# Kernel tuning notes

Hardware: AMD Instinct MI355X
Metric: run time of the kernel (lower is better)

Reference implementation:

```python
import jax, jax.numpy as jnp
import numpy as np

N = 50000          # num graph nodes
E = 800000         # edges per direction
NGRAM, ODIM = 4, 32
DIMS = [128, 128, 64]
CLASSES = 128
MAXPE = 10
L2_EPS = 1e-12


def setup_inputs() -> dict:
    key = jax.random.key(0)
    ks = iter(jax.random.split(key, 40))
    d = {}
    d['x'] = jax.random.normal(next(ks), (N, DIMS[0]), jnp.float32)
    d['edge_index_in'] = jax.random.randint(next(ks), (2, E), 0, N, dtype=jnp.int64)
    d['edge_weight_in'] = jax.random.uniform(next(ks), (E,), jnp.float32)
    d['edge_index_out'] = jax.random.randint(next(ks), (2, E), 0, N, dtype=jnp.int64)
    d['edge_weight_out'] = jax.random.uniform(next(ks), (E,), jnp.float32)
    d['pe_table'] = jax.random.normal(next(ks), (MAXPE, ODIM), jnp.float32) * 0.05
    # per-layer DirectGCNLayer params (weights stored [in,out], i.e. torch W.T)
    for l in range(2):
        di, do = DIMS[l], DIMS[l + 1]
        s = 1.0 / np.sqrt(di)
        d[f'W_main_in_{l}'] = jax.random.normal(next(ks), (di, do), jnp.float32) * s
        d[f'W_main_out_{l}'] = jax.random.normal(next(ks), (di, do), jnp.float32) * s
        d[f'W_shared_{l}'] = jax.random.normal(next(ks), (di, do), jnp.float32) * s
        d[f'b_main_in_{l}'] = jnp.zeros((do,), jnp.float32)
        d[f'b_main_out_{l}'] = jnp.zeros((do,), jnp.float32)
        d[f'b_shared_in_{l}'] = jnp.zeros((do,), jnp.float32)
        d[f'b_shared_out_{l}'] = jnp.zeros((do,), jnp.float32)
        d[f'C_in_{l}'] = jnp.ones((N, 1), jnp.float32)
        d[f'C_out_{l}'] = jnp.ones((N, 1), jnp.float32)
    # residual projection for layer 1 (128 -> 64); layer 0 is identity
    d['res_W_1'] = jax.random.normal(next(ks), (DIMS[1], DIMS[2]), jnp.float32) * (1.0 / np.sqrt(DIMS[1]))
    d['res_b_1'] = jnp.zeros((DIMS[2],), jnp.float32)
    d['dec_W'] = jax.random.normal(next(ks), (DIMS[2], CLASSES), jnp.float32) * (1.0 / np.sqrt(DIMS[2]))
    d['dec_b'] = jnp.zeros((CLASSES,), jnp.float32)
    return d


def _prop(xW, ei, ew):
    # gather source, scale by edge weight, scatter-add to target (PyG aggr='add')
    return jax.ops.segment_sum(ew[:, None] * xW[ei[0]], ei[1], num_segments=N)


def _layer(h, ei_in, ew_in, ei_out, ew_out,
           Wmi, Wmo, Ws, bmi, bmo, bsi, bso, cin, cout):
    xs = h @ Ws  # shared transform, propagated over both edge sets
    ic = _prop(h @ Wmi, ei_in, ew_in) + bmi + _prop(xs, ei_in, ew_in) + bsi
    oc = _prop(h @ Wmo, ei_out, ew_out) + bmo + _prop(xs, ei_out, ew_out) + bso
    return cin * ic + cout * oc


def reference(x, edge_index_in, edge_weight_in, edge_index_out, edge_weight_out,
              pe_table,
              W_main_in_0, W_main_out_0, W_shared_0, b_main_in_0, b_main_out_0,
              b_shared_in_0, b_shared_out_0, C_in_0, C_out_0,
              W_main_in_1, W_main_out_1, W_shared_1, b_main_in_1, b_main_out_1,
              b_shared_in_1, b_shared_out_1, C_in_1, C_out_1,
              res_W_1, res_b_1, dec_W, dec_b):
    # positional encoding: add pe[:n_gram_len] to each n-gram slot
    h = (x.reshape(N, NGRAM, ODIM) + pe_table[:NGRAM][None]).reshape(N, NGRAM * ODIM)
    # layer 0 (identity residual); dropout p=0 / eval -> no-op
    h = jnp.tanh(_layer(h, edge_index_in, edge_weight_in, edge_index_out, edge_weight_out,
                        W_main_in_0, W_main_out_0, W_shared_0, b_main_in_0, b_main_out_0,
                        b_shared_in_0, b_shared_out_0, C_in_0, C_out_0) + h)
    # layer 1 (linear residual projection 128 -> 64)
    h = jnp.tanh(_layer(h, edge_index_in, edge_weight_in, edge_index_out, edge_weight_out,
                        W_main_in_1, W_main_out_1, W_shared_1, b_main_in_1, b_main_out_1,
                        b_shared_in_1, b_shared_out_1, C_in_1, C_out_1)
                 + h @ res_W_1 + res_b_1)
    logits = h @ dec_W + dec_b
    logp = jax.nn.log_softmax(logits, axis=-1)
    emb = h / (jnp.linalg.norm(h, axis=1, keepdims=True) + L2_EPS)
    return logp, emb
```

## Files before the change

kernel.cpp:

```cpp
#include <hip/hip_runtime.h>
#include <hip/hip_bf16.h>
#include <math.h>

typedef __hip_bfloat16  bf16;
typedef __hip_bfloat162 bf162;
typedef __attribute__((ext_vector_type(8))) short short8;
typedef __attribute__((ext_vector_type(4))) float floatx4;

#define BSZ     128
#define NBMAX   512
#define PACHUNK 8192

__device__ inline float4 bf4_to_f4(uint2 v) {
  float2 lo = __bfloat1622float2(*(bf162*)&v.x);
  float2 hi = __bfloat1622float2(*(bf162*)&v.y);
  return make_float4(lo.x, lo.y, hi.x, hi.y);
}
__device__ inline uint2 f4_to_bf4(float4 v) {
  bf162 lo = __float22bfloat162_rn(make_float2(v.x, v.y));
  bf162 hi = __float22bfloat162_rn(make_float2(v.z, v.w));
  uint2 r;
  r.x = *(unsigned*)&lo;
  r.y = *(unsigned*)&hi;
  return r;
}

__global__ __launch_bounds__(256) void k_bhist(const int* __restrict__ eiIn, const int* __restrict__ eiOut,
                                               int E, int* __restrict__ bcnt, int NB) {
  __shared__ int h[NBMAX];
  const int t = threadIdx.x;
  const int set = blockIdx.y;
  const int* dst = (set ? eiOut : eiIn) + E;
  for (int i = t; i < NB; i += 256) h[i] = 0;
  __syncthreads();
  const int base = blockIdx.x * PACHUNK;
  const int m = min(PACHUNK, E - base);
  #pragma unroll 4
  for (int r = 0; r < PACHUNK / 256; ++r) {
    int i = r * 256 + t;
    if (i < m) atomicAdd(&h[dst[base + i] >> 7], 1);
  }
  __syncthreads();
  for (int i = t; i < NB; i += 256) {
    int c = h[i];
    if (c) atomicAdd(&bcnt[set * NBMAX + i], c);
  }
}

__global__ __launch_bounds__(64) void k_bscan(const int* __restrict__ bcnt,
                                              int* __restrict__ BO, int* __restrict__ bcur, int NB) {
  const int set = blockIdx.x;
  const int t = threadIdx.x;
  int carry = 0;
  for (int base = 0; base < NB; base += 64) {
    int idx = base + t;
    int v = (idx < NB) ? bcnt[set * NBMAX + idx] : 0;
    int incl = v;
    #pragma unroll
    for (int d = 1; d < 64; d <<= 1) {
      int u = __shfl_up(incl, d, 64);
      if (t >= d) incl += u;
    }
    if (idx < NB) {
      int e = carry + incl - v;
      BO[set * NBMAX + idx]   = e;
      bcur[set * NBMAX + idx] = e;
    }
    carry += __shfl(incl, 63, 64);
  }
}

__global__ __launch_bounds__(256) void k_partA(const int* __restrict__ eiIn, const float* __restrict__ ewIn,
                                               const int* __restrict__ eiOut, const float* __restrict__ ewOut,
                                               int E, int* __restrict__ bucketCur,
                                               int2* __restrict__ sI, int2* __restrict__ sO, int NB) {
  __shared__ int2 staged[PACHUNK];
  __shared__ int cnt[NBMAX];
  __shared__ int sb[NBMAX];
  const int t = threadIdx.x;
  const int set = blockIdx.y;
  const int*   ei = set ? eiOut : eiIn;
  const float* ew = set ? ewOut : ewIn;
  int2* stg  = set ? sO : sI;
  int*  bcur = bucketCur + set * NBMAX;
  const int base = blockIdx.x * PACHUNK;
  const int m = min(PACHUNK, E - base);
  for (int b = t; b < NB; b += 256) cnt[b] = 0;
  __syncthreads();
  #pragma unroll 4
  for (int r = 0; r < PACHUNK / 256; ++r) {
    int i = r * 256 + t;
    if (i < m) atomicAdd(&cnt[ei[E + base + i] >> 7], 1);
  }
  __syncthreads();
  if (t < 64) {
    int carry = 0;
    int nch = (NB + 63) >> 6;
    for (int c = 0; c < nch; ++c) {
      int idx = c * 64 + t;
      int v = (idx < NB) ? cnt[idx] : 0;
      int incl = v;
      #pragma unroll
      for (int d = 1; d < 64; d <<= 1) {
        int u = __shfl_up(incl, d, 64);
        if (t >= d) incl += u;
      }
      if (idx < NB) sb[idx] = carry + incl - v;
      carry += __shfl(incl, 63, 64);
    }
  }
  __syncthreads();
  for (int b = t; b < NB; b += 256) {
    int c = cnt[b];
    if (c > 0) cnt[b] = atomicAdd(&bcur[b], c) - sb[b];
  }
  __syncthreads();
  #pragma unroll 4
  for (int r = 0; r < PACHUNK / 256; ++r) {
    int i = r * 256 + t;
    if (i < m) {
      int src = ei[base + i];
      int dst = ei[E + base + i];
      float w = ew[base + i];
      int b = dst >> 7;
      int rank = atomicAdd(&sb[b], 1);
      staged[rank] = make_int2(src | ((dst & 127) << 16) | (b << 23), __float_as_int(w));
    }
  }
  __syncthreads();
  #pragma unroll 4
  for (int r = 0; r < PACHUNK / 256; ++r) {
    int j = r * 256 + t;
    if (j < m) {
      int2 p = staged[j];
      int b = ((unsigned)p.x) >> 23;
      stg[cnt[b] + j] = p;
    }
  }
}

__global__ __launch_bounds__(256) void k_partB(const int* __restrict__ BO, const int* __restrict__ bcur,
                                               const int2* __restrict__ sI, const int2* __restrict__ sO,
                                               int2* __restrict__ eI, int2* __restrict__ eO,
                                               int* __restrict__ offsI, int* __restrict__ offsO, int N) {
  __shared__ int cnt[BSZ];
  __shared__ int excl[BSZ];
  __shared__ int cur[BSZ];
  const int t = threadIdx.x;
  const int b = blockIdx.x;
  const int set = blockIdx.y;
  const int2* stg = set ? sO : sI;
  int2* out = set ? eO : eI;
  int*  offs = set ? offsO : offsI;
  const int nlo = b << 7;
  const int nodes = min(BSZ, N - nlo);
  const int lo = BO[set * NBMAX + b];
  const int hi = bcur[set * NBMAX + b];
  if (t < BSZ) cnt[t] = 0;
  __syncthreads();
  for (int i = lo + t; i < hi; i += 256) atomicAdd(&cnt[(stg[i].x >> 16) & 127], 1);
  __syncthreads();
  if (t < 64) {
    int v0 = cnt[t];
    int i0 = v0;
    #pragma unroll
    for (int d = 1; d < 64; d <<= 1) { int u = __shfl_up(i0, d, 64); if (t >= d) i0 += u; }
    int v1 = cnt[64 + t];
    int i1 = v1;
    #pragma unroll
    for (int d = 1; d < 64; d <<= 1) { int u = __shfl_up(i1, d, 64); if (t >= d) i1 += u; }
    int tot0 = __shfl(i0, 63, 64);
    excl[t]      = i0 - v0;
    excl[64 + t] = tot0 + i1 - v1;
  }
  __syncthreads();
  if (t < BSZ) cur[t] = lo + excl[t];
  if (t < nodes) offs[nlo + t] = lo + excl[t];
  if (b == gridDim.x - 1 && t == 0) offs[N] = hi;
  __syncthreads();
  for (int i = lo + t; i < hi; i += 256) {
    int2 p = stg[i];
    int dl = (p.x >> 16) & 127;
    int pos = atomicAdd(&cur[dl], 1);
    out[pos] = make_int2(p.x & 0xffff, p.y);
  }
}

__device__ inline void pack_one(const float* __restrict__ W, bf16* __restrict__ P,
                                int id, int NT, int DO) {
  int lane = id & 63;
  int tile = id >> 6;
  int nt = tile % NT, kt = tile / NT;
  int col  = nt * 16 + (lane & 15);
  int krow = kt * 32 + (lane >> 4) * 8;
  bf16* dst = P + (size_t)id * 8;
  #pragma unroll
  for (int j = 0; j < 8; ++j) dst[j] = __float2bfloat16(W[(size_t)(krow + j) * DO + col]);
}
__global__ void k_packall(const float* __restrict__ Wmi0, const float* __restrict__ Wmo0,
                          const float* __restrict__ Ws0,
                          const float* __restrict__ Wmi1, const float* __restrict__ Wmo1,
                          const float* __restrict__ Ws1,
                          const float* __restrict__ resW, const float* __restrict__ Wd,
                          const float* __restrict__ bmi0, const float* __restrict__ bsi0,
                          const float* __restrict__ bmo0, const float* __restrict__ bso0,
                          const float* __restrict__ bmi1, const float* __restrict__ bsi1,
                          const float* __restrict__ bmo1, const float* __restrict__ bso1,
                          bf16* __restrict__ P0, bf16* __restrict__ P1, bf16* __restrict__ Pd,
                          float* __restrict__ bi0, float* __restrict__ bo0,
                          float* __restrict__ bi1, float* __restrict__ bo1) {
  int id = blockIdx.x * blockDim.x + threadIdx.x;
  const int T0 = 8 * 8 * 64;
  const int T1 = 4 * 12 * 64;
  const int Td = 2 * 8 * 64;
  if (id < T0) {
    int lane = id & 63, tile = id >> 6;
    int nt = tile % 8, kt = tile / 8;
    int col  = nt * 16 + (lane & 15);
    int krow = kt * 32 + (lane >> 4) * 8;
    bf16* dst = P0 + (size_t)id * 8;
    #pragma unroll
    for (int j = 0; j < 8; ++j) {
      int r = krow + j;
      float v = (r < 128 ? Wmi0[r * 128 + col] : Wmo0[(r - 128) * 128 + col])
              + Ws0[(r & 127) * 128 + col];
      dst[j] = __float2bfloat16(v);
    }
  } else if (id < T0 + T1) {
    int id1 = id - T0;
    int lane = id1 & 63, tile = id1 >> 6;
    int nt = tile % 12, kt = tile / 12;
    int col  = nt * 16 + (lane & 15);
    int krow = kt * 32 + (lane >> 4) * 8;
    bf16* dst = P1 + (size_t)id1 * 8;
    #pragma unroll
    for (int j = 0; j < 8; ++j) {
      int k = krow + j;
      float v;
      if (col < 64)       v = Wmi1[k * 64 + col]       + Ws1[k * 64 + col];
      else if (col < 128) v = Wmo1[k * 64 + col - 64]  + Ws1[k * 64 + col - 64];
      else                v = resW[k * 64 + col - 128];
      dst[j] = __float2bfloat16(v);
    }
  } else if (id < T0 + T1 + Td) {
    pack_one(Wd, Pd, id - T0 - T1, 8, 128);
  } else {
    int j = id - (T0 + T1 + Td);
    if (j < 128) { bi0[j] = bmi0[j] + bsi0[j]; bo0[j] = bmo0[j] + bso0[j]; }
    if (j < 64)  { bi1[j] = bmi1[j] + bsi1[j]; bo1[j] = bmo1[j] + bso1[j]; }
  }
}

__global__ void k_prep0(const float* __restrict__ x, const float* __restrict__ pe,
                        bf16* __restrict__ h0, int total) {
  int i = blockIdx.x * blockDim.x + threadIdx.x;
  if (i < total) h0[i] = __float2bfloat16(x[i] + pe[i & 127]);
}

__global__ __launch_bounds__(256) void k_agg0(const bf16* __restrict__ tb,
                                              const int* __restrict__ offsI, const int2* __restrict__ eI,
                                              const int* __restrict__ offsO, const int2* __restrict__ eO,
                                              const float* __restrict__ cin, const float* __restrict__ cou,
                                              bf16* __restrict__ aggC, int N) {
  int n = (blockIdx.x * blockDim.x + threadIdx.x) >> 6;
  int lane = threadIdx.x & 63;
  if (n >= N) return;
  const int dir = lane >> 5;
  const int sub = (lane >> 4) & 1;
  const int sl  = lane & 15;
  const int*   offs = dir ? offsO : offsI;
  const int2*  el   = dir ? eO : eI;
  const float* cc   = dir ? cou : cin;
  const char* base = (const char*)tb + sl * 16;
  float a0 = 0, a1 = 0, a2 = 0, a3 = 0, a4 = 0, a5 = 0, a6 = 0, a7 = 0;
  const int s0 = offs[n], s1 = offs[n + 1];
  int i = s0 + sub;
  if (i + 6 < s1) {
    int2 eA = el[i], eB = el[i + 2], eC = el[i + 4], eD = el[i + 6];
    for (;;) {
      uint4 vA = *(const uint4*)(base + ((size_t)(unsigned)eA.x << 8));
      uint4 vB = *(const uint4*)(base + ((size_t)(unsigned)eB.x << 8));
      uint4 vC = *(const uint4*)(base + ((size_t)(unsigned)eC.x << 8));
      uint4 vD = *(const uint4*)(base + ((size_t)(unsigned)eD.x << 8));
      const bool more = (i + 14 < s1);
      int2 nA, nB, nC, nD;
      if (more) { nA = el[i + 8]; nB = el[i + 10]; nC = el[i + 12]; nD = el[i + 14]; }
      float wA = __int_as_float(eA.y), wB = __int_as_float(eB.y);
      float wC = __int_as_float(eC.y), wD = __int_as_float(eD.y);
      float4 Al = bf4_to_f4(make_uint2(vA.x, vA.y)), Ah = bf4_to_f4(make_uint2(vA.z, vA.w));
      float4 Bl = bf4_to_f4(make_uint2(vB.x, vB.y)), Bh = bf4_to_f4(make_uint2(vB.z, vB.w));
      float4 Cl = bf4_to_f4(make_uint2(vC.x, vC.y)), Ch = bf4_to_f4(make_uint2(vC.z, vC.w));
      float4 Dl = bf4_to_f4(make_uint2(vD.x, vD.y)), Dh = bf4_to_f4(make_uint2(vD.z, vD.w));
      a0 += wA * Al.x + wB * Bl.x + wC * Cl.x + wD * Dl.x;
      a1 += wA * Al.y + wB * Bl.y + wC * Cl.y + wD * Dl.y;
      a2 += wA * Al.z + wB * Bl.z + wC * Cl.z + wD * Dl.z;
      a3 += wA * Al.w + wB * Bl.w + wC * Cl.w + wD * Dl.w;
      a4 += wA * Ah.x + wB * Bh.x + wC * Ch.x + wD * Dh.x;
      a5 += wA * Ah.y + wB * Bh.y + wC * Ch.y + wD * Dh.y;
      a6 += wA * Ah.z + wB * Bh.z + wC * Ch.z + wD * Dh.z;
      a7 += wA * Ah.w + wB * Bh.w + wC * Ch.w + wD * Dh.w;
      i += 8;
      if (!more) break;
      eA = nA; eB = nB; eC = nC; eD = nD;
    }
  }
  for (; i < s1; i += 2) {
    int2 e = el[i];
    uint4 v = *(const uint4*)(base + ((size_t)(unsigned)e.x << 8));
    float w = __int_as_float(e.y);
    float4 lo = bf4_to_f4(make_uint2(v.x, v.y)), hi = bf4_to_f4(make_uint2(v.z, v.w));
    a0 += w * lo.x; a1 += w * lo.y; a2 += w * lo.z; a3 += w * lo.w;
    a4 += w * hi.x; a5 += w * hi.y; a6 += w * hi.z; a7 += w * hi.w;
  }
  a0 += __shfl_xor(a0, 16, 64); a1 += __shfl_xor(a1, 16, 64);
  a2 += __shfl_xor(a2, 16, 64); a3 += __shfl_xor(a3, 16, 64);
  a4 += __shfl_xor(a4, 16, 64); a5 += __shfl_xor(a5, 16, 64);
  a6 += __shfl_xor(a6, 16, 64); a7 += __shfl_xor(a7, 16, 64);
  if (sub == 0) {
    float c = cc[n];
    uint2 plo = f4_to_bf4(make_float4(c * a0, c * a1, c * a2, c * a3));
    uint2 phi = f4_to_bf4(make_float4(c * a4, c * a5, c * a6, c * a7));
    *(uint4*)(aggC + (size_t)n * 256 + dir * 128 + sl * 8) = make_uint4(plo.x, plo.y, phi.x, phi.y);
  }
}

__global__ __launch_bounds__(256) void k_mf0(const bf16* __restrict__ A,
                                             const bf16* __restrict__ Wp,
                                             const float* __restrict__ bi, const float* __restrict__ bo,
                                             const float* __restrict__ cin, const float* __restrict__ cou,
                                             const bf16* __restrict__ h0,
                                             bf16* __restrict__ h1, int N) {
  const int lane = threadIdx.x & 63;
  const int quad = lane >> 4, lc = lane & 15;
  const int bmw = blockIdx.x * 64 + (threadIdx.x >> 6) * 16;
  const int rowc = min(bmw + lc, N - 1);
  const bf16* ap = A + (size_t)rowc * 256 + quad * 8;
  const short8* bp = (const short8*)Wp + lane;
  floatx4 acc[8] = {};
  #pragma unroll
  for (int kt = 0; kt < 8; ++kt) {
    short8 af = *(const short8*)(ap + kt * 32);
    #pragma unroll
    for (int nt = 0; nt < 8; ++nt) {
      short8 bfr = bp[(kt * 8 + nt) * 64];
      acc[nt] = __builtin_amdgcn_mfma_f32_16x16x32_bf16(af, bfr, acc[nt], 0, 0, 0);
    }
  }
  float bif[8], bof[8];
  #pragma unroll
  for (int nt = 0; nt < 8; ++nt) {
    bif[nt] = bi[nt * 16 + lc];
    bof[nt] = bo[nt * 16 + lc];
  }
  #pragma unroll
  for (int r = 0; r < 4; ++r) {
    int gm = bmw + quad * 4 + r;
    if (gm < N) {
      float ci = cin[gm], co = cou[gm];
      #pragma unroll
      for (int nt = 0; nt < 8; ++nt) {
        int col = nt * 16 + lc;
        float v = acc[nt][r] + ci * bif[nt] + co * bof[nt]
                + __bfloat162float(h0[(size_t)gm * 128 + col]);
        h1[(size_t)gm * 128 + col] = __float2bfloat16(tanhf(v));
      }
    }
  }
}

__global__ __launch_bounds__(256) void k_mf1(const bf16* __restrict__ A,
                                             const bf16* __restrict__ Wp,
                                             bf16* __restrict__ t1g, bf16* __restrict__ t1r, int N) {
  const int lane = threadIdx.x & 63;
  const int quad = lane >> 4, lc = lane & 15;
  const int bmw = blockIdx.x * 64 + (threadIdx.x >> 6) * 16;
  const int rowc = min(bmw + lc, N - 1);
  const bf16* ap = A + (size_t)rowc * 128 + quad * 8;
  const short8* bp = (const short8*)Wp + lane;
  floatx4 acc[12] = {};
  #pragma unroll
  for (int kt = 0; kt < 4; ++kt) {
    short8 af = *(const short8*)(ap + kt * 32);
    #pragma unroll
    for (int nt = 0; nt < 12; ++nt) {
      short8 bfr = bp[(kt * 12 + nt) * 64];
      acc[nt] = __builtin_amdgcn_mfma_f32_16x16x32_bf16(af, bfr, acc[nt], 0, 0, 0);
    }
  }
  #pragma unroll
  for (int r = 0; r < 4; ++r) {
    int gm = bmw + quad * 4 + r;
    if (gm < N) {
      #pragma unroll
      for (int nt = 0; nt < 12; ++nt) {
        int col = nt * 16 + lc;
        bf16 v = __float2bfloat16(acc[nt][r]);
        if (col < 128) t1g[(size_t)gm * 128 + col]        = v;
        else           t1r[(size_t)gm * 64 + (col - 128)] = v;
      }
    }
  }
}

__global__ __launch_bounds__(256) void k_agg1(const bf16* __restrict__ t1g, const bf16* __restrict__ t1r,
                                              const int* __restrict__ offsI, const int2* __restrict__ eI,
                                              const int* __restrict__ offsO, const int2* __restrict__ eO,
                                              const float* __restrict__ bi, const float* __restrict__ bo,
                                              const float* __restrict__ resb,
                                              const float* __restrict__ cin, const float* __restrict__ cou,
                                              bf16* __restrict__ h2b, float* __restrict__ emb, int N) {
  int n = (blockIdx.x * blockDim.x + threadIdx.x) >> 6;
  int lane = threadIdx.x & 63;
  if (n >= N) return;
  const int dir = lane >> 5;
  const int sub = (lane >> 3) & 3;
  const int sl  = lane & 7;
  const int*   offs = dir ? offsO : offsI;
  const int2*  el   = dir ? eO : eI;
  const char* base = (const char*)t1g + dir * 128 + sl * 16;
  float a0 = 0, a1 = 0, a2 = 0, a3 = 0, a4 = 0, a5 = 0, a6 = 0, a7 = 0;
  const int s0 = offs[n], s1 = offs[n + 1];
  int i = s0 + sub;
  if (i + 12 < s1) {
    int2 eA = el[i], eB = el[i + 4], eC = el[i + 8], eD = el[i + 12];
    for (;;) {
      uint4 vA = *(const uint4*)(base + ((size_t)(unsigned)eA.x << 8));
      uint4 vB = *(const uint4*)(base + ((size_t)(unsigned)eB.x << 8));
      uint4 vC = *(const uint4*)(base + ((size_t)(unsigned)eC.x << 8));
      uint4 vD = *(const uint4*)(base + ((size_t)(unsigned)eD.x << 8));
      const bool more = (i + 28 < s1);
      int2 nA, nB, nC, nD;
      if (more) { nA = el[i + 16]; nB = el[i + 20]; nC = el[i + 24]; nD = el[i + 28]; }
      float wA = __int_as_float(eA.y), wB = __int_as_float(eB.y);
      float wC = __int_as_float(eC.y), wD = __int_as_float(eD.y);
      float4 Al = bf4_to_f4(make_uint2(vA.x, vA.y)), Ah = bf4_to_f4(make_uint2(vA.z, vA.w));
      float4 Bl = bf4_to_f4(make_uint2(vB.x, vB.y)), Bh = bf4_to_f4(make_uint2(vB.z, vB.w));
      float4 Cl = bf4_to_f4(make_uint2(vC.x, vC.y)), Ch = bf4_to_f4(make_uint2(vC.z, vC.w));
      float4 Dl = bf4_to_f4(make_uint2(vD.x, vD.y)), Dh = bf4_to_f4(make_uint2(vD.z, vD.w));
      a0 += wA * Al.x + wB * Bl.x + wC * Cl.x + wD * Dl.x;
      a1 += wA * Al.y + wB * Bl.y + wC * Cl.y + wD * Dl.y;
      a2 += wA * Al.z + wB * Bl.z + wC * Cl.z + wD * Dl.z;
      a3 += wA * Al.w + wB * Bl.w + wC * Cl.w + wD * Dl.w;
      a4 += wA * Ah.x + wB * Bh.x + wC * Ch.x + wD * Dh.x;
      a5 += wA * Ah.y + wB * Bh.y + wC * Ch.y + wD * Dh.y;
      a6 += wA * Ah.z + wB * Bh.z + wC * Ch.z + wD * Dh.z;
      a7 += wA * Ah.w + wB * Bh.w + wC * Ch.w + wD * Dh.w;
      i += 16;
      if (!more) break;
      eA = nA; eB = nB; eC = nC; eD = nD;
    }
  }
  for (; i < s1; i += 4) {
    int2 e = el[i];
    uint4 v = *(const uint4*)(base + ((size_t)(unsigned)e.x << 8));
    float w = __int_as_float(e.y);
    float4 lo = bf4_to_f4(make_uint2(v.x, v.y)), hi = bf4_to_f4(make_uint2(v.z, v.w));
    a0 += w * lo.x; a1 += w * lo.y; a2 += w * lo.z; a3 += w * lo.w;
    a4 += w * hi.x; a5 += w * hi.y; a6 += w * hi.z; a7 += w * hi.w;
  }
  a0 += __shfl_xor(a0, 8, 64);  a1 += __shfl_xor(a1, 8, 64);
  a2 += __shfl_xor(a2, 8, 64);  a3 += __shfl_xor(a3, 8, 64);
  a4 += __shfl_xor(a4, 8, 64);  a5 += __shfl_xor(a5, 8, 64);
  a6 += __shfl_xor(a6, 8, 64);  a7 += __shfl_xor(a7, 8, 64);
  a0 += __shfl_xor(a0, 16, 64); a1 += __shfl_xor(a1, 16, 64);
  a2 += __shfl_xor(a2, 16, 64); a3 += __shfl_xor(a3, 16, 64);
  a4 += __shfl_xor(a4, 16, 64); a5 += __shfl_xor(a5, 16, 64);
  a6 += __shfl_xor(a6, 16, 64); a7 += __shfl_xor(a7, 16, 64);
  float b0 = __shfl_xor(a0, 32, 64), b1 = __shfl_xor(a1, 32, 64);
  float b2 = __shfl_xor(a2, 32, 64), b3 = __shfl_xor(a3, 32, 64);
  float b4 = __shfl_xor(a4, 32, 64), b5 = __shfl_xor(a5, 32, 64);
  float b6 = __shfl_xor(a6, 32, 64), b7 = __shfl_xor(a7, 32, 64);
  if (sub == 0) {
    const int c = sl * 8;
    float ci = cin[n], co = cou[n];
    float s_in[8]  = { dir ? b0 : a0, dir ? b1 : a1, dir ? b2 : a2, dir ? b3 : a3,
                       dir ? b4 : a4, dir ? b5 : a5, dir ? b6 : a6, dir ? b7 : a7 };
    float s_ou[8]  = { dir ? a0 : b0, dir ? a1 : b1, dir ? a2 : b2, dir ? a3 : b3,
                       dir ? a4 : b4, dir ? a5 : b5, dir ? a6 : b6, dir ? a7 : b7 };
    float4 bif0 = *(const float4*)(bi + c),   bif1 = *(const float4*)(bi + c + 4);
    float4 bof0 = *(const float4*)(bo + c),   bof1 = *(const float4*)(bo + c + 4);
    float4 rbf0 = *(const float4*)(resb + c), rbf1 = *(const float4*)(resb + c + 4);
    uint4 rvu = *(const uint4*)((const char*)t1r + (size_t)n * 128 + sl * 16);
    float4 rv0 = bf4_to_f4(make_uint2(rvu.x, rvu.y));
    float4 rv1 = bf4_to_f4(make_uint2(rvu.z, rvu.w));
    float bif[8] = { bif0.x, bif0.y, bif0.z, bif0.w, bif1.x, bif1.y, bif1.z, bif1.w };
    float bof[8] = { bof0.x, bof0.y, bof0.z, bof0.w, bof1.x, bof1.y, bof1.z, bof1.w };
    float rbf[8] = { rbf0.x, rbf0.y, rbf0.z, rbf0.w, rbf1.x, rbf1.y, rbf1.z, rbf1.w };
    float rvf[8] = { rv0.x, rv0.y, rv0.z, rv0.w, rv1.x, rv1.y, rv1.z, rv1.w };
    float v[8];
    float q = 0.f;
    #pragma unroll
    for (int k = 0; k < 8; ++k) {
      v[k] = tanhf(ci * (s_in[k] + bif[k]) + co * (s_ou[k] + bof[k]) + rvf[k] + rbf[k]);
      q += v[k] * v[k];
    }
    q += __shfl_xor(q, 1, 64);
    q += __shfl_xor(q, 2, 64);
    q += __shfl_xor(q, 4, 64);
    if (dir == 0) {
      uint2 plo = f4_to_bf4(make_float4(v[0], v[1], v[2], v[3]));
      uint2 phi = f4_to_bf4(make_float4(v[4], v[5], v[6], v[7]));
      *(uint4*)(h2b + (size_t)n * 64 + c) = make_uint4(plo.x, plo.y, phi.x, phi.y);
    } else {
      float inv = 1.0f / (sqrtf(q) + 1e-12f);
      *(float4*)(emb + (size_t)n * 64 + c)     = make_float4(v[0] * inv, v[1] * inv, v[2] * inv, v[3] * inv);
      *(float4*)(emb + (size_t)n * 64 + c + 4) = make_float4(v[4] * inv, v[5] * inv, v[6] * inv, v[7] * inv);
    }
  }
}

__global__ __launch_bounds__(256) void k_mfd(const bf16* __restrict__ A,
                                             const bf16* __restrict__ Wp,
                                             const float* __restrict__ bd,
                                             float* __restrict__ logp, int N) {
  const int lane = threadIdx.x & 63;
  const int quad = lane >> 4, lc = lane & 15;
  const int bmw = blockIdx.x * 64 + (threadIdx.x >> 6) * 16;
  const int rowc = min(bmw + lc, N - 1);
  const bf16* ap = A + (size_t)rowc * 64 + quad * 8;
  const short8* bp = (const short8*)Wp + lane;
  floatx4 acc[8] = {};
  #pragma unroll
  for (int kt = 0; kt < 2; ++kt) {
    short8 af = *(const short8*)(ap + kt * 32);
    #pragma unroll
    for (int nt = 0; nt < 8; ++nt) {
      short8 bfr = bp[(kt * 8 + nt) * 64];
      acc[nt] = __builtin_amdgcn_mfma_f32_16x16x32_bf16(af, bfr, acc[nt], 0, 0, 0);
    }
  }
  float bdv[8];
  #pragma unroll
  for (int nt = 0; nt < 8; ++nt) bdv[nt] = bd[nt * 16 + lc];
  #pragma unroll
  for (int r = 0; r < 4; ++r) {
    int gm = bmw + quad * 4 + r;
    float v[8];
    #pragma unroll
    for (int nt = 0; nt < 8; ++nt) v[nt] = acc[nt][r] + bdv[nt];
    float m = v[0];
    #pragma unroll
    for (int nt = 1; nt < 8; ++nt) m = fmaxf(m, v[nt]);
    #pragma unroll
    for (int d = 1; d < 16; d <<= 1) m = fmaxf(m, __shfl_xor(m, d, 64));
    float s = 0.f;
    #pragma unroll
    for (int nt = 0; nt < 8; ++nt) s += __expf(v[nt] - m);
    #pragma unroll
    for (int d = 1; d < 16; d <<= 1) s += __shfl_xor(s, d, 64);
    float lse = m + __logf(s);
    if (gm < N) {
      #pragma unroll
      for (int nt = 0; nt < 8; ++nt) logp[(size_t)gm * 128 + nt * 16 + lc] = v[nt] - lse;
    }
  }
}

extern "C" void kernel_launch(void* const* d_in, const int* in_sizes, int n_in,
                              void* d_out, int out_size, void* d_ws, size_t ws_size,
                              hipStream_t stream) {
  const float* x     = (const float*)d_in[0];
  const int*   ei_in = (const int*)d_in[1];
  const float* ew_in = (const float*)d_in[2];
  const int*   ei_ou = (const int*)d_in[3];
  const float* ew_ou = (const float*)d_in[4];
  const float* pe    = (const float*)d_in[5];
  const float* Wmi0  = (const float*)d_in[6];
  const float* Wmo0  = (const float*)d_in[7];
  const float* Wsh0  = (const float*)d_in[8];
  const float* bmi0  = (const float*)d_in[9];
  const float* bmo0  = (const float*)d_in[10];
  const float* bsi0  = (const float*)d_in[11];
  const float* bso0  = (const float*)d_in[12];
  const float* cin0  = (const float*)d_in[13];
  const float* cou0  = (const float*)d_in[14];
  const float* Wmi1  = (const float*)d_in[15];
  const float* Wmo1  = (const float*)d_in[16];
  const float* Wsh1  = (const float*)d_in[17];
  const float* bmi1  = (const float*)d_in[18];
  const float* bmo1  = (const float*)d_in[19];
  const float* bsi1  = (const float*)d_in[20];
  const float* bso1  = (const float*)d_in[21];
  const float* cin1  = (const float*)d_in[22];
  const float* cou1  = (const float*)d_in[23];
  const float* resW  = (const float*)d_in[24];
  const float* resb  = (const float*)d_in[25];
  const float* Wd    = (const float*)d_in[26];
  const float* bd    = (const float*)d_in[27];

  const int N = in_sizes[0] / 128;
  const int E = in_sizes[2];
  const int NB = (N + BSZ - 1) >> 7;

  char* ws = (char*)d_ws;
  size_t off = 0;
  auto alloc = [&](size_t bytes) -> char* {
    off = (off + 255) & ~(size_t)255;
    char* p = ws + off;
    off += bytes;
    return p;
  };
  bf16*  h0bf  = (bf16*)alloc((size_t)N * 128 * 2);
  bf16*  h1bf  = (bf16*)alloc((size_t)N * 128 * 2);
  bf16*  aggC  = (bf16*)alloc((size_t)N * 256 * 2);
  bf16*  h2b   = (bf16*)alloc((size_t)N * 64 * 2);
  bf16*  Wp0   = (bf16*)alloc(256 * 128 * 2);
  bf16*  Wp1   = (bf16*)alloc(128 * 192 * 2);
  bf16*  Wpd   = (bf16*)alloc(64 * 128 * 2);
  float* bi0   = (float*)alloc(128 * 4);
  float* bo0   = (float*)alloc(128 * 4);
  float* bi1   = (float*)alloc(64 * 4);
  float* bo1   = (float*)alloc(64 * 4);
  int*   bcnt  = (int*)alloc((size_t)2 * NBMAX * 4);
  int*   BO    = (int*)alloc((size_t)2 * NBMAX * 4);
  int*   bcur  = (int*)alloc((size_t)2 * NBMAX * 4);
  int*   offsI = (int*)alloc((size_t)(N + 1) * 4);
  int*   offsO = (int*)alloc((size_t)(N + 1) * 4);
  int2*  sI    = (int2*)alloc((size_t)E * 8);
  int2*  sO    = (int2*)alloc((size_t)E * 8);
  int2*  eI    = (int2*)alloc((size_t)E * 8);
  int2*  eO    = (int2*)alloc((size_t)E * 8);
  bf16* t1g = aggC;
  bf16* t1r = t1g + (size_t)N * 128;

  (void)hipMemsetAsync(bcnt, 0, (size_t)2 * NBMAX * 4, stream);

  dim3 gc((E + PACHUNK - 1) / PACHUNK, 2);
  k_bhist<<<gc, 256, 0, stream>>>(ei_in, ei_ou, E, bcnt, NB);
  k_bscan<<<2, 64, 0, stream>>>(bcnt, BO, bcur, NB);
  k_partA<<<gc, 256, 0, stream>>>(ei_in, ew_in, ei_ou, ew_ou, E, bcur, sI, sO, NB);
  dim3 gb(NB, 2);
  k_partB<<<gb, 256, 0, stream>>>(BO, bcur, sI, sO, eI, eO, offsI, offsO, N);
  k_packall<<<(8 * 8 * 64 + 4 * 12 * 64 + 2 * 8 * 64 + 128 + 255) / 256, 256, 0, stream>>>(
      Wmi0, Wmo0, Wsh0, Wmi1, Wmo1, Wsh1, resW, Wd,
      bmi0, bsi0, bmo0, bso0, bmi1, bsi1, bmo1, bso1,
      Wp0, Wp1, Wpd, bi0, bo0, bi1, bo1);
  k_prep0<<<(N * 128 + 255) / 256, 256, 0, stream>>>(x, pe, h0bf, N * 128);

  int ab = (N + 3) / 4;
  int mb = (N + 63) / 64;
  k_agg0<<<ab, 256, 0, stream>>>(h0bf, offsI, eI, offsO, eO, cin0, cou0, aggC, N);
  k_mf0<<<mb, 256, 0, stream>>>(aggC, Wp0, bi0, bo0, cin0, cou0, h0bf, h1bf, N);
  k_mf1<<<mb, 256, 0, stream>>>(h1bf, Wp1, t1g, t1r, N);

  float* logp = (float*)d_out;
  float* emb  = logp + (size_t)N * 128;
  k_agg1<<<ab, 256, 0, stream>>>(t1g, t1r, offsI, eI, offsO, eO, bi1, bo1, resb, cin1, cou1,
                                 h2b, emb, N);
  k_mfd<<<mb, 256, 0, stream>>>(h2b, Wpd, bd, logp, N);
}
```

Baseline: 362.6 us.

## Fuse layer-0 and layer-1 MFMA GEMMs via LDS and use packed float2 gather accumulation

Merges the layer-0 output GEMM (tanh + residual) with the layer-1 transform GEMM into one kernel, staging the tanh'd h1 tile in shared memory in a permuted K order, with the layer-1 weight packing reordered to match. This removes the h1 global write and reread plus one launch. The gather kernels also switch to packed float2 accumulation with shift-based bf16 unpack and drop the manual edge-index prefetch pipelining. That last change may lose some memory-latency hiding.

```diff
diff --git a/kernel.cpp b/kernel.cpp
--- a/kernel.cpp
+++ b/kernel.cpp
@@ -6,6 +6,7 @@
 typedef __hip_bfloat162 bf162;
 typedef __attribute__((ext_vector_type(8))) short short8;
 typedef __attribute__((ext_vector_type(4))) float floatx4;
+typedef __attribute__((ext_vector_type(2))) float floatx2;
 
 #define BSZ     128
 #define NBMAX   512
@@ -22,6 +23,12 @@
   uint2 r;
   r.x = *(unsigned*)&lo;
   r.y = *(unsigned*)&hi;
+  return r;
+}
+__device__ inline floatx2 bf2_to_f2(unsigned u) {
+  floatx2 r;
+  r.x = __uint_as_float(u << 16);
+  r.y = __uint_as_float(u & 0xffff0000u);
   return r;
 }
 
@@ -235,7 +242,8 @@
     bf16* dst = P1 + (size_t)id1 * 8;
     #pragma unroll
     for (int j = 0; j < 8; ++j) {
-      int k = krow + j;
+      int kp = krow + j;
+      int k = ((kp & 7) << 4) + (kp >> 3);
       float v;
       if (col < 64)       v = Wmi1[k * 64 + col]       + Ws1[k * 64 + col];
       else if (col < 128) v = Wmo1[k * 64 + col - 64]  + Ws1[k * 64 + col - 64];
@@ -272,46 +280,35 @@
   const int2*  el   = dir ? eO : eI;
   const float* cc   = dir ? cou : cin;
   const char* base = (const char*)tb + sl * 16;
-  float a0 = 0, a1 = 0, a2 = 0, a3 = 0, a4 = 0, a5 = 0, a6 = 0, a7 = 0;
+  floatx2 A0 = {0.f, 0.f}, A1 = {0.f, 0.f}, A2 = {0.f, 0.f}, A3 = {0.f, 0.f};
   const int s0 = offs[n], s1 = offs[n + 1];
   int i = s0 + sub;
-  if (i + 6 < s1) {
+  for (; i + 6 < s1; i += 8) {
     int2 eA = el[i], eB = el[i + 2], eC = el[i + 4], eD = el[i + 6];
-    for (;;) {
-      uint4 vA = *(const uint4*)(base + ((size_t)(unsigned)eA.x << 8));
-      uint4 vB = *(const uint4*)(base + ((size_t)(unsigned)eB.x << 8));
-      uint4 vC = *(const uint4*)(base + ((size_t)(unsigned)eC.x << 8));
-      uint4 vD = *(const uint4*)(base + ((size_t)(unsigned)eD.x << 8));
-      const bool more = (i + 14 < s1);
-      int2 nA, nB, nC, nD;
-      if (more) { nA = el[i + 8]; nB = el[i + 10]; nC = el[i + 12]; nD = el[i + 14]; }
-      float wA = __int_as_float(eA.y), wB = __int_as_float(eB.y);
-      float wC = __int_as_float(eC.y), wD = __int_as_float(eD.y);
-      float4 Al = bf4_to_f4(make_uint2(vA.x, vA.y)), Ah = bf4_to_f4(make_uint2(vA.z, vA.w));
-      float4 Bl = bf4_to_f4(make_uint2(vB.x, vB.y)), Bh = bf4_to_f4(make_uint2(vB.z, vB.w));
-      float4 Cl = bf4_to_f4(make_uint2(vC.x, vC.y)), Ch = bf4_to_f4(make_uint2(vC.z, vC.w));
-      float4 Dl = bf4_to_f4(make_uint2(vD.x, vD.y)), Dh = bf4_to_f4(make_uint2(vD.z, vD.w));
-      a0 += wA * Al.x + wB * Bl.x + wC * Cl.x + wD * Dl.x;
-      a1 += wA * Al.y + wB * Bl.y + wC * Cl.y + wD * Dl.y;
-      a2 += wA * Al.z + wB * Bl.z + wC * Cl.z + wD * Dl.z;
-      a3 += wA * Al.w + wB * Bl.w + wC * Cl.w + wD * Dl.w;
-      a4 += wA * Ah.x + wB * Bh.x + wC * Ch.x + wD * Dh.x;
-      a5 += wA * Ah.y + wB * Bh.y + wC * Ch.y + wD * Dh.y;
-      a6 += wA * Ah.z + wB * Bh.z + wC * Ch.z + wD * Dh.z;
-      a7 += wA * Ah.w + wB * Bh.w + wC * Ch.w + wD * Dh.w;
-      i += 8;
-      if (!more) break;
-      eA = nA; eB = nB; eC = nC; eD = nD;
-    }
+    uint4 vA = *(const uint4*)(base + ((size_t)(unsigned)eA.x << 8));
+    uint4 vB = *(const uint4*)(base + ((size_t)(unsigned)eB.x << 8));
+    uint4 vC = *(const uint4*)(base + ((size_t)(unsigned)eC.x << 8));
+    uint4 vD = *(const uint4*)(base + ((size_t)(unsigned)eD.x << 8));
+    float fA = __int_as_float(eA.y), fB = __int_as_float(eB.y);
+    float fC = __int_as_float(eC.y), fD = __int_as_float(eD.y);
+    floatx2 wA = {fA, fA}, wB = {fB, fB}, wC = {fC, fC}, wD = {fD, fD};
+    A0 += wA * bf2_to_f2(vA.x) + wB * bf2_to_f2(vB.x) + wC * bf2_to_f2(vC.x) + wD * bf2_to_f2(vD.x);
+    A1 += wA * bf2_to_f2(vA.y) + wB * bf2_to_f2(vB.y) + wC * bf2_to_f2(vC.y) + wD * bf2_to_f2(vD.y);
+    A2 += wA * bf2_to_f2(vA.z) + wB * bf2_to_f2(vB.z) + wC * bf2_to_f2(vC.z) + wD * bf2_to_f2(vD.z);
+    A3 += wA * bf2_to_f2(vA.w) + wB * bf2_to_f2(vB.w) + wC * bf2_to_f2(vC.w) + wD * bf2_to_f2(vD.w);
   }
   for (; i < s1; i += 2) {
     int2 e = el[i];
     uint4 v = *(const uint4*)(base + ((size_t)(unsigned)e.x << 8));
-    float w = __int_as_float(e.y);
-    float4 lo = bf4_to_f4(make_uint2(v.x, v.y)), hi = bf4_to_f4(make_uint2(v.z, v.w));
-    a0 += w * lo.x; a1 += w * lo.y; a2 += w * lo.z; a3 += w * lo.w;
-    a4 += w * hi.x; a5 += w * hi.y; a6 += w * hi.z; a7 += w * hi.w;
-  }
+    float f = __int_as_float(e.y);
+    floatx2 w2 = {f, f};
+    A0 += w2 * bf2_to_f2(v.x);
+    A1 += w2 * bf2_to_f2(v.y);
+    A2 += w2 * bf2_to_f2(v.z);
+    A3 += w2 * bf2_to_f2(v.w);
+  }
+  float a0 = A0.x, a1 = A0.y, a2 = A1.x, a3 = A1.y;
+  float a4 = A2.x, a5 = A2.y, a6 = A3.x, a7 = A3.y;
   a0 += __shfl_xor(a0, 16, 64); a1 += __shfl_xor(a1, 16, 64);
   a2 += __shfl_xor(a2, 16, 64); a3 += __shfl_xor(a3, 16, 64);
   a4 += __shfl_xor(a4, 16, 64); a5 += __shfl_xor(a5, 16, 64);
@@ -324,18 +321,21 @@
   }
 }
 
-__global__ __launch_bounds__(256) void k_mf0(const bf16* __restrict__ A,
-                                             const bf16* __restrict__ Wp,
-                                             const float* __restrict__ bi, const float* __restrict__ bo,
-                                             const float* __restrict__ cin, const float* __restrict__ cou,
-                                             const bf16* __restrict__ h0,
-                                             bf16* __restrict__ h1, int N) {
+__global__ __launch_bounds__(256) void k_mf01(const bf16* __restrict__ A,
+                                              const bf16* __restrict__ Wp0,
+                                              const bf16* __restrict__ Wp1,
+                                              const float* __restrict__ bi, const float* __restrict__ bo,
+                                              const float* __restrict__ cin, const float* __restrict__ cou,
+                                              const bf16* __restrict__ h0,
+                                              bf16* __restrict__ t1g, bf16* __restrict__ t1r, int N) {
+  __shared__ bf16 hs[64][136];
   const int lane = threadIdx.x & 63;
+  const int wid  = threadIdx.x >> 6;
   const int quad = lane >> 4, lc = lane & 15;
-  const int bmw = blockIdx.x * 64 + (threadIdx.x >> 6) * 16;
+  const int bmw = blockIdx.x * 64 + wid * 16;
   const int rowc = min(bmw + lc, N - 1);
   const bf16* ap = A + (size_t)rowc * 256 + quad * 8;
-  const short8* bp = (const short8*)Wp + lane;
+  const short8* bp = (const short8*)Wp0 + lane;
   floatx4 acc[8] = {};
   #pragma unroll
   for (int kt = 0; kt < 8; ++kt) {
@@ -354,37 +354,31 @@
   }
   #pragma unroll
   for (int r = 0; r < 4; ++r) {
-    int gm = bmw + quad * 4 + r;
-    if (gm < N) {
-      float ci = cin[gm], co = cou[gm];
-      #pragma unroll
-      for (int nt = 0; nt < 8; ++nt) {
-        int col = nt * 16 + lc;
-        float v = acc[nt][r] + ci * bif[nt] + co * bof[nt]
-                + __bfloat162float(h0[(size_t)gm * 128 + col]);
-        h1[(size_t)gm * 128 + col] = __float2bfloat16(tanhf(v));
-      }
-    }
-  }
-}
-
-__global__ __launch_bounds__(256) void k_mf1(const bf16* __restrict__ A,
-                                             const bf16* __restrict__ Wp,
-                                             bf16* __restrict__ t1g, bf16* __restrict__ t1r, int N) {
-  const int lane = threadIdx.x & 63;
-  const int quad = lane >> 4, lc = lane & 15;
-  const int bmw = blockIdx.x * 64 + (threadIdx.x >> 6) * 16;
-  const int rowc = min(bmw + lc, N - 1);
-  const bf16* ap = A + (size_t)rowc * 128 + quad * 8;
-  const short8* bp = (const short8*)Wp + lane;
-  floatx4 acc[12] = {};
+    int gmc = min(bmw + quad * 4 + r, N - 1);
+    float ci = cin[gmc], co = cou[gmc];
+    unsigned hp[4];
+    #pragma unroll
+    for (int np = 0; np < 4; ++np) {
+      int n0 = 2 * np, n1 = 2 * np + 1;
+      float v0 = acc[n0][r] + ci * bif[n0] + co * bof[n0]
+               + __bfloat162float(h0[(size_t)gmc * 128 + n0 * 16 + lc]);
+      float v1 = acc[n1][r] + ci * bif[n1] + co * bof[n1]
+               + __bfloat162float(h0[(size_t)gmc * 128 + n1 * 16 + lc]);
+      bf162 p = __float22bfloat162_rn(make_float2(tanhf(v0), tanhf(v1)));
+      hp[np] = *(unsigned*)&p;
+    }
+    *(uint4*)(&hs[wid * 16 + quad * 4 + r][lc * 8]) = make_uint4(hp[0], hp[1], hp[2], hp[3]);
+  }
+  __syncthreads();
+  const short8* bp1 = (const short8*)Wp1 + lane;
+  floatx4 acc2[12] = {};
   #pragma unroll
   for (int kt = 0; kt < 4; ++kt) {
-    short8 af = *(const short8*)(ap + kt * 32);
+    short8 af = *(const short8*)(&hs[wid * 16 + lc][kt * 32 + quad * 8]);
     #pragma unroll
     for (int nt = 0; nt < 12; ++nt) {
-      short8 bfr = bp[(kt * 12 + nt) * 64];
-      acc[nt] = __builtin_amdgcn_mfma_f32_16x16x32_bf16(af, bfr, acc[nt], 0, 0, 0);
+      short8 bfr = bp1[(kt * 12 + nt) * 64];
+      acc2[nt] = __builtin_amdgcn_mfma_f32_16x16x32_bf16(af, bfr, acc2[nt], 0, 0, 0);
     }
   }
   #pragma unroll
@@ -394,7 +388,7 @@
       #pragma unroll
       for (int nt = 0; nt < 12; ++nt) {
         int col = nt * 16 + lc;
-        bf16 v = __float2bfloat16(acc[nt][r]);
+        bf16 v = __float2bfloat16(acc2[nt][r]);
         if (col < 128) t1g[(size_t)gm * 128 + col]        = v;
         else           t1r[(size_t)gm * 64 + (col - 128)] = v;
       }
@@ -418,46 +412,35 @@
   const int*   offs = dir ? offsO : offsI;
   const int2*  el   = dir ? eO : eI;
   const char* base = (const char*)t1g + dir * 128 + sl * 16;
-  float a0 = 0, a1 = 0, a2 = 0, a3 = 0, a4 = 0, a5 = 0, a6 = 0, a7 = 0;
+  floatx2 A0 = {0.f, 0.f}, A1 = {0.f, 0.f}, A2 = {0.f, 0.f}, A3 = {0.f, 0.f};
   const int s0 = offs[n], s1 = offs[n + 1];
   int i = s0 + sub;
-  if (i + 12 < s1) {
+  for (; i + 12 < s1; i += 16) {
     int2 eA = el[i], eB = el[i + 4], eC = el[i + 8], eD = el[i + 12];
-    for (;;) {
-      uint4 vA = *(const uint4*)(base + ((size_t)(unsigned)eA.x << 8));
-      uint4 vB = *(const uint4*)(base + ((size_t)(unsigned)eB.x << 8));
-      uint4 vC = *(const uint4*)(base + ((size_t)(unsigned)eC.x << 8));
-      uint4 vD = *(const uint4*)(base + ((size_t)(unsigned)eD.x << 8));
-      const bool more = (i + 28 < s1);
-      int2 nA, nB, nC, nD;
-      if (more) { nA = el[i + 16]; nB = el[i + 20]; nC = el[i + 24]; nD = el[i + 28]; }
-      float wA = __int_as_float(eA.y), wB = __int_as_float(eB.y);
-      float wC = __int_as_float(eC.y), wD = __int_as_float(eD.y);
-      float4 Al = bf4_to_f4(make_uint2(vA.x, vA.y)), Ah = bf4_to_f4(make_uint2(vA.z, vA.w));
-      float4 Bl = bf4_to_f4(make_uint2(vB.x, vB.y)), Bh = bf4_to_f4(make_uint2(vB.z, vB.w));
-      float4 Cl = bf4_to_f4(make_uint2(vC.x, vC.y)), Ch = bf4_to_f4(make_uint2(vC.z, vC.w));
-      float4 Dl = bf4_to_f4(make_uint2(vD.x, vD.y)), Dh = bf4_to_f4(make_uint2(vD.z, vD.w));
-      a0 += wA * Al.x + wB * Bl.x + wC * Cl.x + wD * Dl.x;
-      a1 += wA * Al.y + wB * Bl.y + wC * Cl.y + wD * Dl.y;
-      a2 += wA * Al.z + wB * Bl.z + wC * Cl.z + wD * Dl.z;
-      a3 += wA * Al.w + wB * Bl.w + wC * Cl.w + wD * Dl.w;
-      a4 += wA * Ah.x + wB * Bh.x + wC * Ch.x + wD * Dh.x;
-      a5 += wA * Ah.y + wB * Bh.y + wC * Ch.y + wD * Dh.y;
-      a6 += wA * Ah.z + wB * Bh.z + wC * Ch.z + wD * Dh.z;
-      a7 += wA * Ah.w + wB * Bh.w + wC * Ch.w + wD * Dh.w;
-      i += 16;
-      if (!more) break;
-      eA = nA; eB = nB; eC = nC; eD = nD;
-    }
+    uint4 vA = *(const uint4*)(base + ((size_t)(unsigned)eA.x << 8));
+    uint4 vB = *(const uint4*)(base + ((size_t)(unsigned)eB.x << 8));
+    uint4 vC = *(const uint4*)(base + ((size_t)(unsigned)eC.x << 8));
+    uint4 vD = *(const uint4*)(base + ((size_t)(unsigned)eD.x << 8));
+    float fA = __int_as_float(eA.y), fB = __int_as_float(eB.y);
+    float fC = __int_as_float(eC.y), fD = __int_as_float(eD.y);
+    floatx2 wA = {fA, fA}, wB = {fB, fB}, wC = {fC, fC}, wD = {fD, fD};
+    A0 += wA * bf2_to_f2(vA.x) + wB * bf2_to_f2(vB.x) + wC * bf2_to_f2(vC.x) + wD * bf2_to_f2(vD.x);
+    A1 += wA * bf2_to_f2(vA.y) + wB * bf2_to_f2(vB.y) + wC * bf2_to_f2(vC.y) + wD * bf2_to_f2(vD.y);
+    A2 += wA * bf2_to_f2(vA.z) + wB * bf2_to_f2(vB.z) + wC * bf2_to_f2(vC.z) + wD * bf2_to_f2(vD.z);
+    A3 += wA * bf2_to_f2(vA.w) + wB * bf2_to_f2(vB.w) + wC * bf2_to_f2(vC.w) + wD * bf2_to_f2(vD.w);
   }
   for (; i < s1; i += 4) {
     int2 e = el[i];
     uint4 v = *(const uint4*)(base + ((size_t)(unsigned)e.x << 8));
-    float w = __int_as_float(e.y);
-    float4 lo = bf4_to_f4(make_uint2(v.x, v.y)), hi = bf4_to_f4(make_uint2(v.z, v.w));
-    a0 += w * lo.x; a1 += w * lo.y; a2 += w * lo.z; a3 += w * lo.w;
-    a4 += w * hi.x; a5 += w * hi.y; a6 += w * hi.z; a7 += w * hi.w;
-  }
+    float f = __int_as_float(e.y);
+    floatx2 w2 = {f, f};
+    A0 += w2 * bf2_to_f2(v.x);
+    A1 += w2 * bf2_to_f2(v.y);
+    A2 += w2 * bf2_to_f2(v.z);
+    A3 += w2 * bf2_to_f2(v.w);
+  }
+  float a0 = A0.x, a1 = A0.y, a2 = A1.x, a3 = A1.y;
+  float a4 = A2.x, a5 = A2.y, a6 = A3.x, a7 = A3.y;
   a0 += __shfl_xor(a0, 8, 64);  a1 += __shfl_xor(a1, 8, 64);
   a2 += __shfl_xor(a2, 8, 64);  a3 += __shfl_xor(a3, 8, 64);
   a4 += __shfl_xor(a4, 8, 64);  a5 += __shfl_xor(a5, 8, 64);
@@ -601,7 +584,6 @@
     return p;
   };
   bf16*  h0bf  = (bf16*)alloc((size_t)N * 128 * 2);
-  bf16*  h1bf  = (bf16*)alloc((size_t)N * 128 * 2);
   bf16*  aggC  = (bf16*)alloc((size_t)N * 256 * 2);
   bf16*  h2b   = (bf16*)alloc((size_t)N * 64 * 2);
   bf16*  Wp0   = (bf16*)alloc(256 * 128 * 2);
@@ -640,8 +622,7 @@
   int ab = (N + 3) / 4;
   int mb = (N + 63) / 64;
   k_agg0<<<ab, 256, 0, stream>>>(h0bf, offsI, eI, offsO, eO, cin0, cou0, aggC, N);
-  k_mf0<<<mb, 256, 0, stream>>>(aggC, Wp0, bi0, bo0, cin0, cou0, h0bf, h1bf, N);
-  k_mf1<<<mb, 256, 0, stream>>>(h1bf, Wp1, t1g, t1r, N);
+  k_mf01<<<mb, 256, 0, stream>>>(aggC, Wp0, Wp1, bi0, bo0, cin0, cou0, h0bf, t1g, t1r, N);
 
   float* logp = (float*)d_out;
   float* emb  = logp + (size_t)N * 128;
```

Result: faster. 350.3 us (-3.4%).
